# Optimization experiments

Measured on AMD Instinct MI355X. Metric: run time of the kernel, lower is better.

The kernel has to match this reference:

```python
import jax, jax.numpy as jnp
import numpy as np

START_IDX = 1  # Offsets.GO
END_IDX = 2    # Offsets.EOS
NEG_INF = -10000.0


def setup_inputs() -> dict:
    key = jax.random.key(0)
    k1, k2, k3 = jax.random.split(key, 3)
    B, T, N = 256, 1024, 128
    unary = jax.random.normal(k1, (B, T, N), dtype=jnp.float32)
    trans = jax.random.normal(k2, (1, N, N), dtype=jnp.float32) * 0.1
    lengths = jax.random.randint(k3, (B,), 1, T + 1)
    return {"unary": unary, "trans": trans, "lengths": lengths}


def _forward_alg(unary_btn, trans, lengths):
    """CRF log-partition. unary_btn: [B,T,N], trans: [1,N,N], lengths: [B] -> [B]."""
    B, T, N = unary_btn.shape
    tr = trans[0]  # [N(cur), N(prev)]
    unary_tbn = jnp.transpose(unary_btn, (1, 0, 2))  # batch_first -> [T,B,N]

    init_alphas = jnp.full((B, N), NEG_INF, dtype=unary_btn.dtype)
    init_alphas = init_alphas.at[:, START_IDX].set(0.0)

    def step(alphas, inp):
        unary_t, t = inp  # unary_t: [B,N]
        # scores[b, i, j] = alphas[b, j] + trans[i, j] + unary_t[b, i]
        scores = alphas[:, None, :] + tr[None, :, :] + unary_t[:, :, None]
        new_alphas = jax.nn.logsumexp(scores, axis=2)  # [B,N]
        # only advance positions still inside the sequence
        alphas = jnp.where((t < lengths)[:, None], new_alphas, alphas)
        return alphas, None

    alphas, _ = jax.lax.scan(step, init_alphas, (unary_tbn, jnp.arange(T)))
    terminal = alphas + tr[END_IDX][None, :]  # trans[:, end_idx] row: [N]
    return jax.nn.logsumexp(terminal, axis=1)  # [B]


def reference(unary, trans, lengths):
    return _forward_alg(unary, trans, lengths)
```

## Files before the change

kernel.cpp:

```cpp
#include <hip/hip_runtime.h>

#define T_LEN 1024
#define NS    128
#define BT    16
#define G     16
#define SEG   32
#define SSH   5
#define NB    256

typedef __attribute__((ext_vector_type(8))) short short8;
typedef __attribute__((ext_vector_type(4))) short short4v;
typedef __attribute__((ext_vector_type(4))) float f32x4;

static __device__ __forceinline__ short f2bf(float f) {
    unsigned u = __builtin_bit_cast(unsigned, f);
    u = (u + 0x7fffu + ((u >> 16) & 1u)) >> 16;
    return (short)u;
}
static __device__ __forceinline__ float bf2f(short s) {
    unsigned u = ((unsigned)(unsigned short)s) << 16;
    return __builtin_bit_cast(float, u);
}
static __device__ __forceinline__ short f2bf_trunc(float f) {
    return (short)(__builtin_bit_cast(unsigned, f) >> 16);
}

__global__ __launch_bounds__(256, 4) void crf_seg(
        const float* __restrict__ unary, const float* __restrict__ trans,
        const int* __restrict__ lengths,
        float* __restrict__ yv, float* __restrict__ zv,
        float* __restrict__ cfv, float* __restrict__ cbv) {
    __shared__ __align__(16) short Fs[2][BT * NS];
    __shared__ int tbS[BT], teS[BT];
    __shared__ int itersS;

    const int tid = threadIdx.x;
    const int g = blockIdx.x & (G - 1);
    const int u = blockIdx.x >> 4;
    const bool bwd = u >= (SEG - 1);
    const int s = bwd ? (u - (SEG - 2)) : u;
    const int w = tid >> 6, lane = tid & 63;
    const int quad = lane >> 4, bcol = lane & 15;
    const int sr = tid >> 4, sc = tid & 15;

    if (tid == 0) itersS = 0;
    if (tid < BT) {
        int L = lengths[g * BT + tid];
        tbS[tid] = (s * L) >> SSH;
        teS[tid] = ((s + 1) * L) >> SSH;
    }
    __syncthreads();
    if (tid < BT) atomicMax(&itersS, teS[tid] - tbS[tid]);

    const int tb = tbS[bcol], te = teS[bcol];
    const int nrec = te - tb - 1;
    const int s_tb = tbS[sr], s_te = teS[sr];

    short8 Ea[2][4];
    #pragma unroll
    for (int mt = 0; mt < 2; ++mt) {
        const int i = w * 32 + mt * 16 + bcol;
        #pragma unroll
        for (int kt = 0; kt < 4; ++kt) {
            short8 e;
            if (!bwd) {
                const float* tr = trans + (size_t)i * NS + kt * 32 + quad * 8;
                float4 x = *(const float4*)tr, y = *(const float4*)(tr + 4);
                e[0] = f2bf(__expf(x.x)); e[1] = f2bf(__expf(x.y));
                e[2] = f2bf(__expf(x.z)); e[3] = f2bf(__expf(x.w));
                e[4] = f2bf(__expf(y.x)); e[5] = f2bf(__expf(y.y));
                e[6] = f2bf(__expf(y.z)); e[7] = f2bf(__expf(y.w));
            } else {
                #pragma unroll
                for (int jj = 0; jj < 8; ++jj)
                    e[jj] = f2bf(__expf(trans[(size_t)(kt * 32 + quad * 8 + jj) * NS + i]));
            }
            Ea[mt][kt] = e;
        }
    }

    {
        const float* ubase = unary + (size_t)(g * BT + sr) * T_LEN * NS + sc * 8;
        float v[8];
        if (!bwd) {
            #pragma unroll
            for (int k = 0; k < 8; ++k)
                v[k] = (s == 0) ? ((sc * 8 + k == 1) ? 1.f : 0.f) : 1.f;
        } else {
            int ti = s_te - 1; if (ti < 0) ti = 0;
            const float* up = ubase + (size_t)ti * NS;
            float4 ua = *(const float4*)up, ub4 = *(const float4*)(up + 4);
            float uu[8] = {ua.x, ua.y, ua.z, ua.w, ub4.x, ub4.y, ub4.z, ub4.w};
            #pragma unroll
            for (int k = 0; k < 8; ++k) {
                float vv = (s == SEG - 1) ? __expf(trans[2 * NS + sc * 8 + k]) : 1.f;
                v[k] = __expf(uu[k]) * vv;
            }
        }
        short8 z;
        #pragma unroll
        for (int k = 0; k < 8; ++k) z[k] = f2bf(v[k]);
        *(short8*)&Fs[0][sr * NS + ((sc ^ sr) << 3)] = z;

        if (s_te == s_tb) {
            if (!bwd) {
                float* yp = yv + ((size_t)s * NB + g * BT + sr) * NS + sc * 8;
                #pragma unroll
                for (int k = 0; k < 8; ++k)
                    yp[k] = (s == 0) ? ((sc * 8 + k == 1) ? 1.f : 0.f) : 1.f;
                if (sc == 0) cfv[s * NB + g * BT + sr] = 0.f;
            } else {
                float* zp = zv + ((size_t)(s - 1) * NB + g * BT + sr) * NS + sc * 8;
                #pragma unroll
                for (int k = 0; k < 8; ++k) zp[k] = 1.f;
                if (sc == 0) cbv[(s - 1) * NB + g * BT + sr] = 0.f;
            }
        }
    }

    const float* uptr = unary + (size_t)(g * BT + bcol) * T_LEN * NS + (w * 32 + quad * 4);
    #define T_OFB(nn) ({ int _t = bwd ? (te - 2 - (nn)) : (tb + (nn)); \
                         _t = _t < 0 ? 0 : (_t > T_LEN - 1 ? T_LEN - 1 : _t); _t; })
    float4 pA0, pA1, pB0, pB1;
    { int t = T_OFB(0);
      pA0 = *(const float4*)(uptr + (size_t)t * NS);
      pA1 = *(const float4*)(uptr + (size_t)t * NS + 16); }
    { int t = T_OFB(1);
      pB0 = *(const float4*)(uptr + (size_t)t * NS);
      pB1 = *(const float4*)(uptr + (size_t)t * NS + 16); }
    __syncthreads();
    const int iters = itersS;

    int bfOff[4];
    #pragma unroll
    for (int kt = 0; kt < 4; ++kt) bfOff[kt] = bcol * NS + (((kt * 4 + quad) ^ bcol) << 3);
    const int s4Off = bcol * NS + (bcol << 3);
    const int c0 = w * 4 + (quad >> 1), half = (quad & 1) << 2;
    const int fw0 = bcol * NS + ((c0 ^ bcol) << 3) + half;
    const int fw1 = bcol * NS + (((c0 + 2) ^ bcol) << 3) + half;

    float C = 0.f;

#define STEP(U0, U1) do {                                                         \
    const int cur = n & 1, nxt = cur ^ 1;                                         \
    const short* fb = Fs[cur];                                                    \
    short8 Bf0 = *(const short8*)&fb[bfOff[0]];                                   \
    short8 Bf1 = *(const short8*)&fb[bfOff[1]];                                   \
    short8 Bf2 = *(const short8*)&fb[bfOff[2]];                                   \
    short8 Bf3 = *(const short8*)&fb[bfOff[3]];                                   \
    short4v s4 = *(const short4v*)&fb[s4Off];                                     \
    float e0[4], e1[4];                                                           \
    e0[0] = __expf(U0.x); e0[1] = __expf(U0.y);                                   \
    e0[2] = __expf(U0.z); e0[3] = __expf(U0.w);                                   \
    e1[0] = __expf(U1.x); e1[1] = __expf(U1.y);                                   \
    e1[2] = __expf(U1.z); e1[3] = __expf(U1.w);                                   \
    { int t = T_OFB(n + 2);                                                       \
      U0 = *(const float4*)(uptr + (size_t)t * NS);                               \
      U1 = *(const float4*)(uptr + (size_t)t * NS + 16); }                        \
    f32x4 x0 = {0.f,0.f,0.f,0.f}, y0 = {0.f,0.f,0.f,0.f};                         \
    f32x4 x1 = {0.f,0.f,0.f,0.f}, y1 = {0.f,0.f,0.f,0.f};                         \
    x0 = __builtin_amdgcn_mfma_f32_16x16x32_bf16(Ea[0][0], Bf0, x0, 0, 0, 0);     \
    x1 = __builtin_amdgcn_mfma_f32_16x16x32_bf16(Ea[1][0], Bf0, x1, 0, 0, 0);     \
    y0 = __builtin_amdgcn_mfma_f32_16x16x32_bf16(Ea[0][2], Bf2, y0, 0, 0, 0);     \
    y1 = __builtin_amdgcn_mfma_f32_16x16x32_bf16(Ea[1][2], Bf2, y1, 0, 0, 0);     \
    x0 = __builtin_amdgcn_mfma_f32_16x16x32_bf16(Ea[0][1], Bf1, x0, 0, 0, 0);     \
    x1 = __builtin_amdgcn_mfma_f32_16x16x32_bf16(Ea[1][1], Bf1, x1, 0, 0, 0);     \
    y0 = __builtin_amdgcn_mfma_f32_16x16x32_bf16(Ea[0][3], Bf3, y0, 0, 0, 0);     \
    y1 = __builtin_amdgcn_mfma_f32_16x16x32_bf16(Ea[1][3], Bf3, y1, 0, 0, 0);     \
    f32x4 a0 = x0 + y0, a1 = x1 + y1;                                             \
    float sv = (bf2f(s4[0]) + bf2f(s4[1])) + (bf2f(s4[2]) + bf2f(s4[3]));         \
    float rs = __fdividef(1.f, sv);                                               \
    float logs = __logf(sv);                                                      \
    float fn0[4], fn1[4];                                                         \
    fn0[0] = a0[0]*e0[0]*rs; fn0[1] = a0[1]*e0[1]*rs;                             \
    fn0[2] = a0[2]*e0[2]*rs; fn0[3] = a0[3]*e0[3]*rs;                             \
    fn1[0] = a1[0]*e1[0]*rs; fn1[1] = a1[1]*e1[1]*rs;                             \
    fn1[2] = a1[2]*e1[2]*rs; fn1[3] = a1[3]*e1[3]*rs;                             \
    if (n == nrec) {                                                              \
        if (!bwd) {              \
            float* yp = yv + ((size_t)s * NB + g * BT + bcol) * NS;               \
            *(float4*)(yp + w * 32 + quad * 4)      = (float4){fn0[0], fn0[1], fn0[2], fn0[3]}; \
            *(float4*)(yp + w * 32 + 16 + quad * 4) = (float4){fn1[0], fn1[1], fn1[2], fn1[3]}; \
            if (tid < BT) cfv[s * NB + g * BT + tid] = C + logs;                  \
        } else {                  \
            float* zp = zv + ((size_t)(s - 1) * NB + g * BT + bcol) * NS;         \
            *(float4*)(zp + w * 32 + quad * 4)      = (float4){a0[0], a0[1], a0[2], a0[3]}; \
            *(float4*)(zp + w * 32 + 16 + quad * 4) = (float4){a1[0], a1[1], a1[2], a1[3]}; \
            if (tid < BT) cbv[(s - 1) * NB + g * BT + tid] = C;                   \
        }                                                                         \
    }                                                                             \
    C += logs;                                                                    \
    short4v p0, p1;                                                               \
    p0[0] = f2bf_trunc(fn0[0]); p0[1] = f2bf_trunc(fn0[1]);                       \
    p0[2] = f2bf_trunc(fn0[2]); p0[3] = f2bf_trunc(fn0[3]);                       \
    p1[0] = f2bf_trunc(fn1[0]); p1[1] = f2bf_trunc(fn1[1]);                       \
    p1[2] = f2bf_trunc(fn1[2]); p1[3] = f2bf_trunc(fn1[3]);                       \
    *(short4v*)&Fs[nxt][fw0] = p0;                                                \
    *(short4v*)&Fs[nxt][fw1] = p1;                                                \
     \
    asm volatile("s_waitcnt lgkmcnt(0)" ::: "memory");                            \
    __builtin_amdgcn_s_barrier();                                                 \
} while (0)

    for (int n = 0; n < iters; ) {
        STEP(pA0, pA1); ++n;
        if (n >= iters) break;
        STEP(pB0, pB1); ++n;
    }
#undef STEP
#undef T_OFB
}

__global__ __launch_bounds__(64) void crf_combine(
        const float* __restrict__ yv, const float* __restrict__ zv,
        const float* __restrict__ cfv, const float* __restrict__ cbv,
        float* __restrict__ out) {
    const int b = blockIdx.x, lane = threadIdx.x;
    float acc = cfv[b];
    for (int s = 1; s <= SEG - 1; ++s) acc += cbv[(s - 1) * NB + b];
    float lg = 0.f;
    for (int s = 1; s <= SEG - 1; ++s) {
        const float* Z = zv + ((size_t)(s - 1) * NB + b) * NS;
        const float* Y = yv + ((size_t)(s - 1) * NB + b) * NS;
        float d = Z[lane] * Y[lane] + Z[lane + 64] * Y[lane + 64];
        #pragma unroll
        for (int off = 1; off < 64; off <<= 1) d += __shfl_xor(d, off, 64);
        lg += __logf(d);
    }
    for (int s = 1; s <= SEG - 2; ++s) {
        const float* Y = yv + ((size_t)s * NB + b) * NS;
        float t = Y[lane] + Y[lane + 64];
        #pragma unroll
        for (int off = 1; off < 64; off <<= 1) t += __shfl_xor(t, off, 64);
        lg -= __logf(t);
    }
    if (lane == 0) out[b] = acc + lg;
}

extern "C" void kernel_launch(void* const* d_in, const int* in_sizes, int n_in,
                              void* d_out, int out_size, void* d_ws, size_t ws_size,
                              hipStream_t stream) {
    const float* unary   = (const float*)d_in[0];
    const float* trans   = (const float*)d_in[1];
    const int*   lengths = (const int*)d_in[2];
    float* out = (float*)d_out;

    float* yv  = (float*)d_ws;
    float* zv  = yv + (size_t)(SEG - 1) * NB * NS;
    float* cfv = zv + (size_t)(SEG - 1) * NB * NS;
    float* cbv = cfv + (size_t)(SEG - 1) * NB;

    crf_seg<<<dim3(2 * (SEG - 1) * G), dim3(256), 0, stream>>>(
        unary, trans, lengths, yv, zv, cfv, cbv);
    crf_combine<<<dim3(NB), dim3(64), 0, stream>>>(yv, zv, cfv, cbv, out);
}
```

Measured before the change: 228.9 us.

## Run each segment block as a single wavefront and drop the LDS double buffer

Each segment block now runs as one 64-lane wavefront instead of four, and that wave computes all 128 output states per step with 32 MFMAs across eight independent accumulators. Segment bounds and the iteration count are now computed per lane, with the max found through cross-lane shuffles, so the shared-memory atomic and the block-level barriers go away. The double-buffered LDS state becomes a single buffer that is updated in place. The cost is a much higher register footprint and only about one wave per SIMD, so LDS and global-load latency now has to be hidden by instruction-level parallelism instead of by other waves.

```diff
diff --git a/kernel.cpp b/kernel.cpp
--- a/kernel.cpp
+++ b/kernel.cpp
@@ -25,41 +25,35 @@
     return (short)(__builtin_bit_cast(unsigned, f) >> 16);
 }
 
-__global__ __launch_bounds__(256, 4) void crf_seg(
+__global__ __launch_bounds__(64, 1) void crf_seg(
         const float* __restrict__ unary, const float* __restrict__ trans,
         const int* __restrict__ lengths,
         float* __restrict__ yv, float* __restrict__ zv,
         float* __restrict__ cfv, float* __restrict__ cbv) {
-    __shared__ __align__(16) short Fs[2][BT * NS];
-    __shared__ int tbS[BT], teS[BT];
-    __shared__ int itersS;
+    __shared__ __align__(16) short Fs[BT * NS];
 
     const int tid = threadIdx.x;
     const int g = blockIdx.x & (G - 1);
     const int u = blockIdx.x >> 4;
     const bool bwd = u >= (SEG - 1);
     const int s = bwd ? (u - (SEG - 2)) : u;
-    const int w = tid >> 6, lane = tid & 63;
-    const int quad = lane >> 4, bcol = lane & 15;
-    const int sr = tid >> 4, sc = tid & 15;
-
-    if (tid == 0) itersS = 0;
-    if (tid < BT) {
-        int L = lengths[g * BT + tid];
-        tbS[tid] = (s * L) >> SSH;
-        teS[tid] = ((s + 1) * L) >> SSH;
-    }
-    __syncthreads();
-    if (tid < BT) atomicMax(&itersS, teS[tid] - tbS[tid]);
-
-    const int tb = tbS[bcol], te = teS[bcol];
+    const int quad = tid >> 4, bcol = tid & 15;
+
+    const int Lb = lengths[g * BT + bcol];
+    const int tb = (s * Lb) >> SSH, te = ((s + 1) * Lb) >> SSH;
     const int nrec = te - tb - 1;
-    const int s_tb = tbS[sr], s_te = teS[sr];
-
-    short8 Ea[2][4];
-    #pragma unroll
-    for (int mt = 0; mt < 2; ++mt) {
-        const int i = w * 32 + mt * 16 + bcol;
+    int dlen = te - tb;
+    #pragma unroll
+    for (int m = 1; m < 16; m <<= 1) {
+        int o = __shfl_xor(dlen, m, 64);
+        dlen = o > dlen ? o : dlen;
+    }
+    const int iters = dlen;
+
+    short8 Ea[8][4];
+    #pragma unroll
+    for (int j = 0; j < 8; ++j) {
+        const int i = j * 16 + bcol;
         #pragma unroll
         for (int kt = 0; kt < 4; ++kt) {
             short8 e;
@@ -75,11 +69,16 @@
                 for (int jj = 0; jj < 8; ++jj)
                     e[jj] = f2bf(__expf(trans[(size_t)(kt * 32 + quad * 8 + jj) * NS + i]));
             }
-            Ea[mt][kt] = e;
+            Ea[j][kt] = e;
         }
     }
 
-    {
+    #pragma unroll
+    for (int rep = 0; rep < 4; ++rep) {
+        const int tv = rep * 64 + tid;
+        const int sr = tv >> 4, sc = tv & 15;
+        const int Ls = lengths[g * BT + sr];
+        const int s_tb = (s * Ls) >> SSH, s_te = ((s + 1) * Ls) >> SSH;
         const float* ubase = unary + (size_t)(g * BT + sr) * T_LEN * NS + sc * 8;
         float v[8];
         if (!bwd) {
@@ -100,7 +99,7 @@
         short8 z;
         #pragma unroll
         for (int k = 0; k < 8; ++k) z[k] = f2bf(v[k]);
-        *(short8*)&Fs[0][sr * NS + ((sc ^ sr) << 3)] = z;
+        *(short8*)&Fs[sr * NS + ((sc ^ sr) << 3)] = z;
 
         if (s_te == s_tb) {
             if (!bwd) {
@@ -118,94 +117,100 @@
         }
     }
 
-    const float* uptr = unary + (size_t)(g * BT + bcol) * T_LEN * NS + (w * 32 + quad * 4);
+    const float* uptr = unary + (size_t)(g * BT + bcol) * T_LEN * NS + quad * 4;
     #define T_OFB(nn) ({ int _t = bwd ? (te - 2 - (nn)) : (tb + (nn)); \
                          _t = _t < 0 ? 0 : (_t > T_LEN - 1 ? T_LEN - 1 : _t); _t; })
-    float4 pA0, pA1, pB0, pB1;
-    { int t = T_OFB(0);
-      pA0 = *(const float4*)(uptr + (size_t)t * NS);
-      pA1 = *(const float4*)(uptr + (size_t)t * NS + 16); }
-    { int t = T_OFB(1);
-      pB0 = *(const float4*)(uptr + (size_t)t * NS);
-      pB1 = *(const float4*)(uptr + (size_t)t * NS + 16); }
-    __syncthreads();
-    const int iters = itersS;
+    float4 pA[8], pB[8];
+    {
+        int t = T_OFB(0);
+        #pragma unroll
+        for (int j = 0; j < 8; ++j) pA[j] = *(const float4*)(uptr + (size_t)t * NS + j * 16);
+        t = T_OFB(1);
+        #pragma unroll
+        for (int j = 0; j < 8; ++j) pB[j] = *(const float4*)(uptr + (size_t)t * NS + j * 16);
+    }
 
     int bfOff[4];
     #pragma unroll
     for (int kt = 0; kt < 4; ++kt) bfOff[kt] = bcol * NS + (((kt * 4 + quad) ^ bcol) << 3);
     const int s4Off = bcol * NS + (bcol << 3);
-    const int c0 = w * 4 + (quad >> 1), half = (quad & 1) << 2;
-    const int fw0 = bcol * NS + ((c0 ^ bcol) << 3) + half;
-    const int fw1 = bcol * NS + (((c0 + 2) ^ bcol) << 3) + half;
-
+    int fwo[8];
+    #pragma unroll
+    for (int j = 0; j < 8; ++j) {
+        const int cj = 2 * j + (quad >> 1);
+        fwo[j] = bcol * NS + ((cj ^ bcol) << 3) + ((quad & 1) << 2);
+    }
+
+    asm volatile("s_waitcnt lgkmcnt(0)" ::: "memory");
     float C = 0.f;
 
-#define STEP(U0, U1) do {                                                         \
-    const int cur = n & 1, nxt = cur ^ 1;                                         \
-    const short* fb = Fs[cur];                                                    \
-    short8 Bf0 = *(const short8*)&fb[bfOff[0]];                                   \
-    short8 Bf1 = *(const short8*)&fb[bfOff[1]];                                   \
-    short8 Bf2 = *(const short8*)&fb[bfOff[2]];                                   \
-    short8 Bf3 = *(const short8*)&fb[bfOff[3]];                                   \
-    short4v s4 = *(const short4v*)&fb[s4Off];                                     \
-    float e0[4], e1[4];                                                           \
-    e0[0] = __expf(U0.x); e0[1] = __expf(U0.y);                                   \
-    e0[2] = __expf(U0.z); e0[3] = __expf(U0.w);                                   \
-    e1[0] = __expf(U1.x); e1[1] = __expf(U1.y);                                   \
-    e1[2] = __expf(U1.z); e1[3] = __expf(U1.w);                                   \
+#define STEP(U) do {                                                              \
+    short8 Bf0 = *(const short8*)&Fs[bfOff[0]];                                   \
+    short8 Bf1 = *(const short8*)&Fs[bfOff[1]];                                   \
+    short8 Bf2 = *(const short8*)&Fs[bfOff[2]];                                   \
+    short8 Bf3 = *(const short8*)&Fs[bfOff[3]];                                   \
+    short4v s4 = *(const short4v*)&Fs[s4Off];                                     \
+    float e_[8][4];                                                               \
+    _Pragma("unroll")                                                             \
+    for (int j = 0; j < 8; ++j) {                                                 \
+        e_[j][0] = __expf(U[j].x); e_[j][1] = __expf(U[j].y);                     \
+        e_[j][2] = __expf(U[j].z); e_[j][3] = __expf(U[j].w);                     \
+    }                                                                             \
     { int t = T_OFB(n + 2);                                                       \
-      U0 = *(const float4*)(uptr + (size_t)t * NS);                               \
-      U1 = *(const float4*)(uptr + (size_t)t * NS + 16); }                        \
-    f32x4 x0 = {0.f,0.f,0.f,0.f}, y0 = {0.f,0.f,0.f,0.f};                         \
-    f32x4 x1 = {0.f,0.f,0.f,0.f}, y1 = {0.f,0.f,0.f,0.f};                         \
-    x0 = __builtin_amdgcn_mfma_f32_16x16x32_bf16(Ea[0][0], Bf0, x0, 0, 0, 0);     \
-    x1 = __builtin_amdgcn_mfma_f32_16x16x32_bf16(Ea[1][0], Bf0, x1, 0, 0, 0);     \
-    y0 = __builtin_amdgcn_mfma_f32_16x16x32_bf16(Ea[0][2], Bf2, y0, 0, 0, 0);     \
-    y1 = __builtin_amdgcn_mfma_f32_16x16x32_bf16(Ea[1][2], Bf2, y1, 0, 0, 0);     \
-    x0 = __builtin_amdgcn_mfma_f32_16x16x32_bf16(Ea[0][1], Bf1, x0, 0, 0, 0);     \
-    x1 = __builtin_amdgcn_mfma_f32_16x16x32_bf16(Ea[1][1], Bf1, x1, 0, 0, 0);     \
-    y0 = __builtin_amdgcn_mfma_f32_16x16x32_bf16(Ea[0][3], Bf3, y0, 0, 0, 0);     \
-    y1 = __builtin_amdgcn_mfma_f32_16x16x32_bf16(Ea[1][3], Bf3, y1, 0, 0, 0);     \
-    f32x4 a0 = x0 + y0, a1 = x1 + y1;                                             \
+      _Pragma("unroll")                                                           \
+      for (int j = 0; j < 8; ++j)                                                 \
+          U[j] = *(const float4*)(uptr + (size_t)t * NS + j * 16); }              \
+    f32x4 acc[8];                                                                 \
+    _Pragma("unroll")                                                             \
+    for (int j = 0; j < 8; ++j) acc[j] = (f32x4){0.f, 0.f, 0.f, 0.f};             \
+    _Pragma("unroll")                                                             \
+    for (int j = 0; j < 8; ++j) acc[j] = __builtin_amdgcn_mfma_f32_16x16x32_bf16(Ea[j][0], Bf0, acc[j], 0, 0, 0); \
+    _Pragma("unroll")                                                             \
+    for (int j = 0; j < 8; ++j) acc[j] = __builtin_amdgcn_mfma_f32_16x16x32_bf16(Ea[j][1], Bf1, acc[j], 0, 0, 0); \
+    _Pragma("unroll")                                                             \
+    for (int j = 0; j < 8; ++j) acc[j] = __builtin_amdgcn_mfma_f32_16x16x32_bf16(Ea[j][2], Bf2, acc[j], 0, 0, 0); \
+    _Pragma("unroll")                                                             \
+    for (int j = 0; j < 8; ++j) acc[j] = __builtin_amdgcn_mfma_f32_16x16x32_bf16(Ea[j][3], Bf3, acc[j], 0, 0, 0); \
     float sv = (bf2f(s4[0]) + bf2f(s4[1])) + (bf2f(s4[2]) + bf2f(s4[3]));         \
     float rs = __fdividef(1.f, sv);                                               \
     float logs = __logf(sv);                                                      \
-    float fn0[4], fn1[4];                                                         \
-    fn0[0] = a0[0]*e0[0]*rs; fn0[1] = a0[1]*e0[1]*rs;                             \
-    fn0[2] = a0[2]*e0[2]*rs; fn0[3] = a0[3]*e0[3]*rs;                             \
-    fn1[0] = a1[0]*e1[0]*rs; fn1[1] = a1[1]*e1[1]*rs;                             \
-    fn1[2] = a1[2]*e1[2]*rs; fn1[3] = a1[3]*e1[3]*rs;                             \
+    float fn[8][4];                                                               \
+    _Pragma("unroll")                                                             \
+    for (int j = 0; j < 8; ++j) {                                                 \
+        fn[j][0] = acc[j][0] * e_[j][0] * rs; fn[j][1] = acc[j][1] * e_[j][1] * rs; \
+        fn[j][2] = acc[j][2] * e_[j][2] * rs; fn[j][3] = acc[j][3] * e_[j][3] * rs; \
+    }                                                                             \
     if (n == nrec) {                                                              \
         if (!bwd) {              \
             float* yp = yv + ((size_t)s * NB + g * BT + bcol) * NS;               \
-            *(float4*)(yp + w * 32 + quad * 4)      = (float4){fn0[0], fn0[1], fn0[2], fn0[3]}; \
-            *(float4*)(yp + w * 32 + 16 + quad * 4) = (float4){fn1[0], fn1[1], fn1[2], fn1[3]}; \
+            _Pragma("unroll")                                                     \
+            for (int j = 0; j < 8; ++j)                                           \
+                *(float4*)(yp + j * 16 + quad * 4) = (float4){fn[j][0], fn[j][1], fn[j][2], fn[j][3]}; \
             if (tid < BT) cfv[s * NB + g * BT + tid] = C + logs;                  \
         } else {                  \
             float* zp = zv + ((size_t)(s - 1) * NB + g * BT + bcol) * NS;         \
-            *(float4*)(zp + w * 32 + quad * 4)      = (float4){a0[0], a0[1], a0[2], a0[3]}; \
-            *(float4*)(zp + w * 32 + 16 + quad * 4) = (float4){a1[0], a1[1], a1[2], a1[3]}; \
+            _Pragma("unroll")                                                     \
+            for (int j = 0; j < 8; ++j)                                           \
+                *(float4*)(zp + j * 16 + quad * 4) = (float4){acc[j][0], acc[j][1], acc[j][2], acc[j][3]}; \
             if (tid < BT) cbv[(s - 1) * NB + g * BT + tid] = C;                   \
         }                                                                         \
     }                                                                             \
     C += logs;                                                                    \
-    short4v p0, p1;                                                               \
-    p0[0] = f2bf_trunc(fn0[0]); p0[1] = f2bf_trunc(fn0[1]);                       \
-    p0[2] = f2bf_trunc(fn0[2]); p0[3] = f2bf_trunc(fn0[3]);                       \
-    p1[0] = f2bf_trunc(fn1[0]); p1[1] = f2bf_trunc(fn1[1]);                       \
-    p1[2] = f2bf_trunc(fn1[2]); p1[3] = f2bf_trunc(fn1[3]);                       \
-    *(short4v*)&Fs[nxt][fw0] = p0;                                                \
-    *(short4v*)&Fs[nxt][fw1] = p1;                                                \
-     \
+    _Pragma("unroll")                                                             \
+    for (int j = 0; j < 8; ++j) {                                                 \
+        short4v p;                                                                \
+        p[0] = f2bf_trunc(fn[j][0]); p[1] = f2bf_trunc(fn[j][1]);                 \
+        p[2] = f2bf_trunc(fn[j][2]); p[3] = f2bf_trunc(fn[j][3]);                 \
+        *(short4v*)&Fs[fwo[j]] = p;                                               \
+    }                                                                             \
+                      \
     asm volatile("s_waitcnt lgkmcnt(0)" ::: "memory");                            \
-    __builtin_amdgcn_s_barrier();                                                 \
 } while (0)
 
     for (int n = 0; n < iters; ) {
-        STEP(pA0, pA1); ++n;
+        STEP(pA); ++n;
         if (n >= iters) break;
-        STEP(pB0, pB1); ++n;
+        STEP(pB); ++n;
     }
 #undef STEP
 #undef T_OFB
@@ -250,7 +255,7 @@
     float* cfv = zv + (size_t)(SEG - 1) * NB * NS;
     float* cbv = cfv + (size_t)(SEG - 1) * NB;
 
-    crf_seg<<<dim3(2 * (SEG - 1) * G), dim3(256), 0, stream>>>(
+    crf_seg<<<dim3(2 * (SEG - 1) * G), dim3(64), 0, stream>>>(
         unary, trans, lengths, yv, zv, cfv, cbv);
     crf_combine<<<dim3(NB), dim3(64), 0, stream>>>(yv, zv, cfv, cbv, out);
 }
```

After: 250.4 us. 9.4% more time.
